# Kernel tuning notes

Measured on AMD Instinct MI355X. Metric: run time of the kernel, lower is better.

The kernel has to match this reference:

```python
import jax, jax.numpy as jnp
import numpy as np

B, N = 16384, 2048  # batch, number of digits


def setup_inputs() -> dict:
    key = jax.random.key(0)
    k1, k2 = jax.random.split(key)
    a = jax.random.randint(k1, (B, N), 0, 10).astype(jnp.float32)
    b = jax.random.randint(k2, (B, N), 0, 10).astype(jnp.float32)
    # Fixed weights from RNNAdder.__init__
    w_ih = jnp.ones((2, 2), jnp.float32)                      # rnn.weight_ih_l0
    w_hh = jnp.array([[1.0, -1.0], [1.0, -1.0]], jnp.float32)  # rnn.weight_hh_l0
    b_ih = jnp.zeros((2,), jnp.float32)                       # rnn.bias_ih_l0
    b_hh = jnp.array([-9.0, -10.0], jnp.float32)              # rnn.bias_hh_l0
    w_carry = jnp.array([[1.0, -1.0]], jnp.float32)           # carry_out.weight
    return {"a": a, "b": b, "w_ih": w_ih, "w_hh": w_hh,
            "b_ih": b_ih, "b_hh": b_hh, "w_carry": w_carry}


def reference(a, b, w_ih, w_hh, b_ih, b_hh, w_carry):
    batch, n = a.shape
    # LSB-first digit streams (torch: stack then flip(1))
    a_r = a[:, ::-1]
    b_r = b[:, ::-1]
    x = jnp.stack([a_r, b_r], axis=2)          # (B, N, 2)
    xs = jnp.transpose(x, (1, 0, 2))            # (N, B, 2) time-major for scan

    h_init = jnp.zeros((batch, 2), a.dtype)

    def step(h, xt):
        # Elman RNN cell with relu nonlinearity (batch_first RNN unrolled)
        h_new = jax.nn.relu(xt @ w_ih.T + b_ih + h @ w_hh.T + b_hh)
        return h_new, h_new

    h_fin, h_seq = jax.lax.scan(step, h_init, xs)   # h_fin (B,2), h_seq (N,B,2)

    # carry_out linear (no bias): (N,B,2) @ (2,1) -> (N,B) -> (B,N)
    carry = jnp.moveaxis((h_seq @ w_carry.T)[..., 0], 0, 1)
    carry_prev = jnp.concatenate(
        [jnp.zeros((batch, 1), a.dtype), carry[:, :-1]], axis=1)

    s = a_r + b_r + carry_prev
    digits = jnp.round(s - 10.0 * carry)[:, ::-1].astype(jnp.int32)  # MSB-first
    final_carry = jnp.round(h_fin @ w_carry.T).astype(jnp.int32)     # (B,1)
    return jnp.concatenate([final_carry, digits], axis=1)            # (B, N+1)
```

## Files before the change

### kernel.cpp

```cpp
#include <hip/hip_runtime.h>


#define NDIG 2048
#define TPB 256
#define DPT 8
#define NW (TPB / 64)

__global__ __launch_bounds__(TPB) void rnn_adder_kernel(
    const float* __restrict__ A, const float* __restrict__ B,
    int* __restrict__ out) {
  const int t = threadIdx.x;
  const int lane = t & 63;
  const int wave = t >> 6;
  const int row = blockIdx.x;
  const int base = NDIG - (t + 1) * DPT;

  const float4* A4 = reinterpret_cast<const float4*>(A + (size_t)row * NDIG + base);
  const float4* B4 = reinterpret_cast<const float4*>(B + (size_t)row * NDIG + base);
  float4 a0 = A4[0], a1 = A4[1];
  float4 b0 = B4[0], b1 = B4[1];

  int s[DPT];
  s[0] = (int)(a0.x + b0.x);
  s[1] = (int)(a0.y + b0.y);
  s[2] = (int)(a0.z + b0.z);
  s[3] = (int)(a0.w + b0.w);
  s[4] = (int)(a1.x + b1.x);
  s[5] = (int)(a1.y + b1.y);
  s[6] = (int)(a1.z + b1.z);
  s[7] = (int)(a1.w + b1.w);

  int c0 = 0, c1 = 1;
#pragma unroll
  for (int k = DPT - 1; k >= 0; --k) {
    c0 = ((s[k] + c0 + 22) >> 5) & 1;
    c1 = ((s[k] + c1 + 22) >> 5) & 1;
  }

  int cur = c0 | (c1 << 1);
#pragma unroll
  for (int off = 1; off < 64; off <<= 1) {
    int prev = __shfl_up(cur, off, 64);
    prev = (lane >= off) ? prev : 2;
    cur = ((cur >> (prev & 1)) & 1) | (((cur >> ((prev >> 1) & 1)) & 1) << 1);
  }

  __shared__ int wagg[NW];
  if (lane == 63) wagg[wave] = cur;
  __syncthreads();

  int wc = 0;
  for (int w = 0; w < wave; ++w) wc = (wagg[w] >> wc) & 1;

  int pr = __shfl_up(cur, 1, 64);
  int cin = (lane == 0) ? wc : ((pr >> wc) & 1);

  int c = cin;
#pragma unroll
  for (int k = DPT - 1; k >= 0; --k) {
    int v = s[k] + c;
    c = ((v + 22) >> 5) & 1;
    s[k] = v - 10 * c;
  }

  int* orow = out + (size_t)row * (NDIG + 1);
#pragma unroll
  for (int k = 0; k < DPT; ++k) orow[1 + base + k] = s[k];
  if (t == TPB - 1) orow[0] = c;
}

extern "C" void kernel_launch(void* const* d_in, const int* in_sizes, int n_in,
                              void* d_out, int out_size, void* d_ws, size_t ws_size,
                              hipStream_t stream) {
  const float* A = (const float*)d_in[0];
  const float* B = (const float*)d_in[1];
  int* out = (int*)d_out;
  const int rows = in_sizes[0] / NDIG;
  rnn_adder_kernel<<<rows, TPB, 0, stream>>>(A, B, out);
}
```

Before: 75.24 us.

## Use persistent grid-stride blocks with software-prefetched next-row loads

Launches a capped grid of 2048 blocks that loop over rows, prefetching the next row's inputs into registers while computing the current row's carry scan. Double-buffered shared-memory wave aggregates let consecutive iterations share one barrier each. The goal is to hide global load latency and cut block launch overhead. The cost is more registers and fewer resident blocks than one block per row.

```diff
diff --git a/kernel.cpp b/kernel.cpp
--- a/kernel.cpp
+++ b/kernel.cpp
@@ -5,68 +5,90 @@
 #define TPB 256
 #define DPT 8
 #define NW (TPB / 64)
+#define NBLK 2048
 
 __global__ __launch_bounds__(TPB) void rnn_adder_kernel(
     const float* __restrict__ A, const float* __restrict__ B,
-    int* __restrict__ out) {
+    int* __restrict__ out, int rows) {
   const int t = threadIdx.x;
   const int lane = t & 63;
   const int wave = t >> 6;
-  const int row = blockIdx.x;
+  const int stride = gridDim.x;
   const int base = NDIG - (t + 1) * DPT;
 
-  const float4* A4 = reinterpret_cast<const float4*>(A + (size_t)row * NDIG + base);
-  const float4* B4 = reinterpret_cast<const float4*>(B + (size_t)row * NDIG + base);
-  float4 a0 = A4[0], a1 = A4[1];
-  float4 b0 = B4[0], b1 = B4[1];
+  __shared__ int wagg[2][NW];
 
-  int s[DPT];
-  s[0] = (int)(a0.x + b0.x);
-  s[1] = (int)(a0.y + b0.y);
-  s[2] = (int)(a0.z + b0.z);
-  s[3] = (int)(a0.w + b0.w);
-  s[4] = (int)(a1.x + b1.x);
-  s[5] = (int)(a1.y + b1.y);
-  s[6] = (int)(a1.z + b1.z);
-  s[7] = (int)(a1.w + b1.w);
+  int r = blockIdx.x;
+  if (r >= rows) return;
 
-  int c0 = 0, c1 = 1;
+  const float4* A4 = reinterpret_cast<const float4*>(A + (size_t)r * NDIG + base);
+  const float4* B4 = reinterpret_cast<const float4*>(B + (size_t)r * NDIG + base);
+  float4 a0 = A4[0], a1 = A4[1], b0 = B4[0], b1 = B4[1];
+
+  int par = 0;
+  while (true) {
+    const int rn = r + stride;
+    const bool more = rn < rows;
+    float4 na0, na1, nb0, nb1;
+    if (more) {
+      const float4* nA4 = reinterpret_cast<const float4*>(A + (size_t)rn * NDIG + base);
+      const float4* nB4 = reinterpret_cast<const float4*>(B + (size_t)rn * NDIG + base);
+      na0 = nA4[0]; na1 = nA4[1]; nb0 = nB4[0]; nb1 = nB4[1];
+    }
+
+    int s[DPT];
+    s[0] = (int)(a0.x + b0.x);
+    s[1] = (int)(a0.y + b0.y);
+    s[2] = (int)(a0.z + b0.z);
+    s[3] = (int)(a0.w + b0.w);
+    s[4] = (int)(a1.x + b1.x);
+    s[5] = (int)(a1.y + b1.y);
+    s[6] = (int)(a1.z + b1.z);
+    s[7] = (int)(a1.w + b1.w);
+
+    int c0 = 0, c1 = 1;
 #pragma unroll
-  for (int k = DPT - 1; k >= 0; --k) {
-    c0 = ((s[k] + c0 + 22) >> 5) & 1;
-    c1 = ((s[k] + c1 + 22) >> 5) & 1;
+    for (int k = DPT - 1; k >= 0; --k) {
+      c0 = ((s[k] + c0 + 22) >> 5) & 1;
+      c1 = ((s[k] + c1 + 22) >> 5) & 1;
+    }
+
+    int cur = c0 | (c1 << 1);
+#pragma unroll
+    for (int off = 1; off < 64; off <<= 1) {
+      int prev = __shfl_up(cur, off, 64);
+      prev = (lane >= off) ? prev : 2;
+      cur = ((cur >> (prev & 1)) & 1) | (((cur >> ((prev >> 1) & 1)) & 1) << 1);
+    }
+
+    if (lane == 63) wagg[par][wave] = cur;
+    __syncthreads();
+    int wc = 0;
+#pragma unroll
+    for (int w = 0; w < NW; ++w)
+      if (w < wave) wc = (wagg[par][w] >> wc) & 1;
+
+    int pr = __shfl_up(cur, 1, 64);
+    int cin = (lane == 0) ? wc : ((pr >> wc) & 1);
+
+    int c = cin;
+#pragma unroll
+    for (int k = DPT - 1; k >= 0; --k) {
+      int v = s[k] + c;
+      c = ((v + 22) >> 5) & 1;
+      s[k] = v - 10 * c;
+    }
+
+    int* orow = out + (size_t)r * (NDIG + 1);
+#pragma unroll
+    for (int k = 0; k < DPT; ++k) orow[1 + base + k] = s[k];
+    if (t == TPB - 1) orow[0] = c;
+
+    if (!more) break;
+    r = rn;
+    par ^= 1;
+    a0 = na0; a1 = na1; b0 = nb0; b1 = nb1;
   }
-
-  int cur = c0 | (c1 << 1);
-#pragma unroll
-  for (int off = 1; off < 64; off <<= 1) {
-    int prev = __shfl_up(cur, off, 64);
-    prev = (lane >= off) ? prev : 2;
-    cur = ((cur >> (prev & 1)) & 1) | (((cur >> ((prev >> 1) & 1)) & 1) << 1);
-  }
-
-  __shared__ int wagg[NW];
-  if (lane == 63) wagg[wave] = cur;
-  __syncthreads();
-
-  int wc = 0;
-  for (int w = 0; w < wave; ++w) wc = (wagg[w] >> wc) & 1;
-
-  int pr = __shfl_up(cur, 1, 64);
-  int cin = (lane == 0) ? wc : ((pr >> wc) & 1);
-
-  int c = cin;
-#pragma unroll
-  for (int k = DPT - 1; k >= 0; --k) {
-    int v = s[k] + c;
-    c = ((v + 22) >> 5) & 1;
-    s[k] = v - 10 * c;
-  }
-
-  int* orow = out + (size_t)row * (NDIG + 1);
-#pragma unroll
-  for (int k = 0; k < DPT; ++k) orow[1 + base + k] = s[k];
-  if (t == TPB - 1) orow[0] = c;
 }
 
 extern "C" void kernel_launch(void* const* d_in, const int* in_sizes, int n_in,
@@ -76,5 +98,6 @@
   const float* B = (const float*)d_in[1];
   int* out = (int*)d_out;
   const int rows = in_sizes[0] / NDIG;
-  rnn_adder_kernel<<<rows, TPB, 0, stream>>>(A, B, out);
+  const int nblk = rows < NBLK ? rows : NBLK;
+  rnn_adder_kernel<<<nblk, TPB, 0, stream>>>(A, B, out, rows);
 }
```

Result: slower. 81.59 us (+8.4%).
